# Optimization experiments

Measured on AMD Instinct MI355X. Metric: run time of the kernel, lower is better.

## Reference

```python
import jax, jax.numpy as jnp
import numpy as np

B, T, D, U = 64, 2048, 256, 256

def hard_sigmoid(x):
    return jnp.clip(0.2 * x + 0.5, 0.0, 1.0)

def setup_inputs() -> dict:
    key = jax.random.key(0)
    k1, k2, k3 = jax.random.split(key, 3)
    x = jax.random.normal(k1, (B, T, D), dtype=jnp.float32)
    kernel = jax.random.normal(k2, (D, 3 * U), dtype=jnp.float32) * (1.0 / np.sqrt(D))
    recurrent_kernel = jax.random.normal(k3, (U, 3 * U), dtype=jnp.float32) * (1.0 / np.sqrt(U))
    bias = jnp.zeros((3 * U,), dtype=jnp.float32)
    return {"x": x, "kernel": kernel, "recurrent_kernel": recurrent_kernel, "bias": bias}

def reference(x, kernel, recurrent_kernel, bias):
    # implementation=0 style: precompute input projections for all timesteps in one big matmul
    # x: [B,T,D], kernel: [D,3U] -> xz/xr/xh each [B,T,U]
    units = recurrent_kernel.shape[0]
    x_proj = jnp.einsum('btd,dh->bth', x, kernel) + bias  # [B,T,3U]
    xz, xr, xh = jnp.split(x_proj, 3, axis=-1)
    Uz = recurrent_kernel[:, :units]
    Ur = recurrent_kernel[:, units:2 * units]
    Uh = recurrent_kernel[:, 2 * units:]

    def step(h, xs):
        xz_t, xr_t, xh_t = xs  # each [B,U]
        z = hard_sigmoid(xz_t + h @ Uz)
        r = hard_sigmoid(xr_t + h @ Ur)
        hh = jnp.tanh(xh_t + (r * h) @ Uh)
        h_new = z * h + (1.0 - z) * hh
        return h_new, None

    h0 = jnp.zeros((x.shape[0], units), dtype=x.dtype)
    # scan over time: move T to leading axis
    xs = (jnp.swapaxes(xz, 0, 1), jnp.swapaxes(xr, 0, 1), jnp.swapaxes(xh, 0, 1))
    h_last, _ = jax.lax.scan(step, h0, xs)
    return h_last  # [B, U] (return_sequences=False)
```

## Files before the change

### kernel.cpp

```cpp
#include <hip/hip_runtime.h>


#define TB 2048
#define NU 256
#define G3 768

typedef __attribute__((ext_vector_type(8))) short bf16x8;
typedef __attribute__((ext_vector_type(4))) float f32x4;

__device__ inline unsigned short f2bf(float f){
  union{float f; unsigned u;} v; v.f = f;
  unsigned r = v.u + 0x7fffu + ((v.u >> 16) & 1u);
  return (unsigned short)(r >> 16);
}
__device__ inline unsigned pk2(float a, float b){
  return (unsigned)f2bf(a) | ((unsigned)f2bf(b) << 16);
}
__device__ inline float bflo(unsigned u){
  union{unsigned u; float f;} v; v.u = u << 16; return v.f;
}
__device__ inline float bfhi(unsigned u){
  union{unsigned u; float f;} v; v.u = u & 0xffff0000u; return v.f;
}
__device__ inline unsigned cvtpk(float a, float b){
  unsigned r;
  asm("v_cvt_pk_bf16_f32 %0, %1, %2" : "=v"(r) : "v"(a), "v"(b));
  return r;
}
__device__ inline float exp2_fast(float x){
#if __has_builtin(__builtin_amdgcn_exp2f)
  return __builtin_amdgcn_exp2f(x);
#else
  float r; asm("v_exp_f32 %0, %1" : "=v"(r) : "v"(x)); return r;
#endif
}

__global__ __launch_bounds__(256) void transpose_k(const float* __restrict__ W,
                                                   const float* __restrict__ R,
                                                   unsigned short* __restrict__ Wt,
                                                   unsigned short* __restrict__ Ut){
  int n = blockIdx.x;
  int k = threadIdx.x;
  if (n < G3) Wt[n*NU + k] = f2bf(W[k*G3 + n]);
  else        Ut[(n-G3)*NU + k] = f2bf(R[k*G3 + (n-G3)]);
}

__global__ __launch_bounds__(256) void proj_k(const float* __restrict__ x,
                                              const unsigned short* __restrict__ Wt,
                                              const float* __restrict__ bias,
                                              unsigned short* __restrict__ XA,
                                              unsigned short* __restrict__ XB){
  __shared__ short As[4096];
  __shared__ short Bs[4096];
  __shared__ short St[4096];
  const int tid  = threadIdx.x;
  const int lane = tid & 63;
  const int wv   = tid >> 6;
  const int wr   = wv >> 1, wc = wv & 1;
  const int q    = lane >> 4, r16 = lane & 15;
  const int tm   = blockIdx.x;
  const int bn   = blockIdx.y;

  f32x4 acc[2][2];
  #pragma unroll
  for (int a=0;a<2;a++)
    #pragma unroll
    for (int b=0;b<2;b++) acc[a][b] = {0.f,0.f,0.f,0.f};

  const int mA = tid >> 2, kq = tid & 3;
  const int kc32 = kq >> 1, q0 = (kq & 1) * 2;

  for (int kc0 = 0; kc0 < 256; kc0 += 64){
    {
      const float* src = x + (size_t)mA*(2048*256) + (size_t)tm*256 + kc0 + kq*16;
      float4 f0 = *(const float4*)(src);
      float4 f1 = *(const float4*)(src+4);
      float4 f2 = *(const float4*)(src+8);
      float4 f3 = *(const float4*)(src+12);
      *(uint2*)&As[kc32*2048 + q0*512     + mA*8 + 0] = make_uint2(pk2(f0.x,f0.y), pk2(f0.z,f0.w));
      *(uint2*)&As[kc32*2048 + q0*512     + mA*8 + 4] = make_uint2(pk2(f1.x,f1.y), pk2(f1.z,f1.w));
      *(uint2*)&As[kc32*2048 + (q0+1)*512 + mA*8 + 0] = make_uint2(pk2(f2.x,f2.y), pk2(f2.z,f2.w));
      *(uint2*)&As[kc32*2048 + (q0+1)*512 + mA*8 + 4] = make_uint2(pk2(f3.x,f3.y), pk2(f3.z,f3.w));
    }
    {
      const unsigned short* srcB = Wt + (size_t)(bn*64 + mA)*256 + kc0 + kq*16;
      uint4 b0v = *(const uint4*)(srcB);
      uint4 b1v = *(const uint4*)(srcB+8);
      *(uint4*)&Bs[kc32*2048 + q0*512     + mA*8] = b0v;
      *(uint4*)&Bs[kc32*2048 + (q0+1)*512 + mA*8] = b1v;
    }
    __syncthreads();
    #pragma unroll
    for (int kk = 0; kk < 2; kk++){
      bf16x8 av[2], bv[2];
      #pragma unroll
      for (int rt=0; rt<2; rt++)
        av[rt] = *(const bf16x8*)&As[kk*2048 + q*512 + (wr*32+rt*16+r16)*8];
      #pragma unroll
      for (int ct=0; ct<2; ct++)
        bv[ct] = *(const bf16x8*)&Bs[kk*2048 + q*512 + (wc*32+ct*16+r16)*8];
      #pragma unroll
      for (int rt=0; rt<2; rt++)
        #pragma unroll
        for (int ct=0; ct<2; ct++)
          acc[rt][ct] = __builtin_amdgcn_mfma_f32_16x16x32_bf16(av[rt], bv[ct], acc[rt][ct], 0,0,0);
    }
    __syncthreads();
  }

  const int csub = (bn < 4) ? 0 : (bn < 8 ? 256 : 512);
  #pragma unroll
  for (int rt=0; rt<2; rt++){
    #pragma unroll
    for (int ct=0; ct<2; ct++){
      int colg = bn*64 + wc*32 + ct*16 + r16;
      float bb = bias[colg];
      int c = colg - csub;
      int wi = (c >> 5) & 1, tt2 = (c >> 4) & 1, r16g = c & 15;
      #pragma unroll
      for (int i=0;i<4;i++){
        int b = wr*32 + rt*16 + q*4 + i;
        int gg = b >> 4, lb = b & 15;
        int lane_ = (lb >> 2)*16 + r16g, ii = lb & 3;
        St[(gg*2+wi)*512 + lane_*8 + tt2*4 + ii] = (short)f2bf(acc[rt][ct][i] + bb);
      }
    }
  }
  __syncthreads();

  #pragma unroll
  for (int it=0; it<2; it++){
    int idx = tid + it*256;
    int chunk = idx >> 6, within = idx & 63;
    int gg = chunk >> 1, wi = chunk & 1;
    int w_ = (bn & 3)*2 + wi;
    uint4 val = *(const uint4*)&St[chunk*512 + within*8];
    if (bn < 8){
      int sel = (bn < 4) ? 0 : 1;
      *((uint4*)XA + ((((size_t)tm*4+gg)*8 + w_)*64 + within)*2 + sel) = val;
    } else {
      *((uint4*)XB + (((size_t)tm*4+gg)*8 + w_)*64 + within) = val;
    }
  }
}

__global__ __launch_bounds__(512, 2) void gru_k(const unsigned short* __restrict__ XA,
                                                const unsigned short* __restrict__ XB,
                                                const unsigned short* __restrict__ Ut,
                                                float* __restrict__ out){
  __shared__ short fb[8192];

  const int tid  = threadIdx.x;
  const int w    = tid >> 6;
  const int lane = tid & 63;
  const int q    = lane >> 4, r16 = lane & 15;
  const int g    = blockIdx.x;
  const int b0   = g * 16;

  const int lswz = (lane & ~3) | ((lane & 3) ^ ((((lane >> 4) & 1) << 1) | ((lane >> 3) & 1)));
  const int ix   = ((r16 >> 3) << 1) | ((lane >> 5) & 1);
  const int wrb  = w*512 + (r16 >> 3)*128 + q*32 + (r16 & 7);

  for (int i = tid; i < 8192; i += 512) fb[i] = 0;

  bf16x8 Uz[2][8], Ur[2][8], Uh[2][8];
  #pragma unroll
  for (int tt=0; tt<2; tt++){
    int cz = w*32 + tt*16 + r16;
    #pragma unroll
    for (int kc=0; kc<8; kc++){
      Uz[tt][kc] = *(const bf16x8*)&Ut[(cz      )*256 + kc*32 + q*8];
      Ur[tt][kc] = *(const bf16x8*)&Ut[(cz + 256)*256 + kc*32 + q*8];
      Uh[tt][kc] = *(const bf16x8*)&Ut[(cz + 512)*256 + kc*32 + q*8];
    }
  }

  float hprev[2][4] = {{0.f,0.f,0.f,0.f},{0.f,0.f,0.f,0.f}};

  const uint4* pA = (const uint4*)XA + ((size_t)(g*8+w)*64 + lane)*2;
  const uint4* pB = (const uint4*)XB + ((size_t)(g*8+w)*64 + lane);

  uint4 xa0 = pA[0], xa1 = pA[1];
  uint4 xb0 = pB[0];
  pA += 4096; pB += 2048;

  __syncthreads();

  #pragma unroll 1
  for (int t = 0; t < TB; t++){
    uint4 na0 = pA[0], na1 = pA[1];
    uint4 nb0 = pB[0];
    pA += 4096; pB += 2048;

    unsigned xw[8] = {xa0.x,xa0.y,xa0.z,xa0.w,xa1.x,xa1.y,xa1.z,xa1.w};

    f32x4 az[2], ar[2];
    #pragma unroll
    for (int tt=0; tt<2; tt++){
      #pragma unroll
      for (int i=0;i<4;i++){
        int s  = tt*4 + i;
        int sr = 8 + s;
        az[tt][i] = (s&1)  ? bfhi(xw[s>>1])  : bflo(xw[s>>1]);
        ar[tt][i] = (sr&1) ? bfhi(xw[sr>>1]) : bflo(xw[sr>>1]);
      }
    }
    #pragma unroll
    for (int kc=0; kc<8; kc++){
      bf16x8 a = *(const bf16x8*)&fb[kc*512 + lswz*8];
      ar[0] = __builtin_amdgcn_mfma_f32_16x16x32_bf16(a, Ur[0][kc], ar[0], 0,0,0);
      ar[1] = __builtin_amdgcn_mfma_f32_16x16x32_bf16(a, Ur[1][kc], ar[1], 0,0,0);
      az[0] = __builtin_amdgcn_mfma_f32_16x16x32_bf16(a, Uz[0][kc], az[0], 0,0,0);
      az[1] = __builtin_amdgcn_mfma_f32_16x16x32_bf16(a, Uz[1][kc], az[1], 0,0,0);
    }
    #pragma unroll
    for (int tt=0; tt<2; tt++){
      #pragma unroll
      for (int i=0;i<4;i++){
        float rr = __builtin_amdgcn_fmed3f(fmaf(0.2f, ar[tt][i], 0.5f), 0.f, 1.f);
        float v  = rr * hprev[tt][i];
        fb[4096 + wrb + tt*256 + ((i^ix)<<3)] = (short)cvtpk(v, v);
      }
    }
    __syncthreads();

    f32x4 ah[2];
    {
      unsigned xwb[4] = {xb0.x,xb0.y,xb0.z,xb0.w};
      #pragma unroll
      for (int ct=0; ct<2; ct++){
        #pragma unroll
        for (int i=0;i<4;i++){
          int s = ct*4 + i;
          ah[ct][i] = (s&1) ? bfhi(xwb[s>>1]) : bflo(xwb[s>>1]);
        }
      }
    }
    #pragma unroll
    for (int kc=0; kc<8; kc++){
      bf16x8 vv = *(const bf16x8*)&fb[4096 + kc*512 + lswz*8];
      ah[0] = __builtin_amdgcn_mfma_f32_16x16x32_bf16(vv, Uh[0][kc], ah[0], 0,0,0);
      ah[1] = __builtin_amdgcn_mfma_f32_16x16x32_bf16(vv, Uh[1][kc], ah[1], 0,0,0);
    }
    float z8[2][4];
    #pragma unroll
    for (int tt=0; tt<2; tt++)
      #pragma unroll
      for (int i=0;i<4;i++)
        z8[tt][i] = __builtin_amdgcn_fmed3f(fmaf(0.2f, az[tt][i], 0.5f), 0.f, 1.f);
    #pragma unroll
    for (int ct=0; ct<2; ct++){
      #pragma unroll
      for (int i=0;i<4;i++){
        float e  = exp2_fast(2.8853900817779268f * ah[ct][i]);
        float rc = __builtin_amdgcn_rcpf(e + 1.f);
        float hh = fmaf(-2.f, rc, 1.f);
        float hn = fmaf(z8[ct][i], hprev[ct][i] - hh, hh);
        hprev[ct][i] = hn;
        fb[wrb + ct*256 + ((i^ix)<<3)] = (short)cvtpk(hn, hn);
      }
    }
    __syncthreads();

    xa0 = na0; xa1 = na1; xb0 = nb0;
  }

  #pragma unroll
  for (int ct=0; ct<2; ct++)
    #pragma unroll
    for (int i=0;i<4;i++)
      out[(size_t)(b0 + q*4 + i)*256 + w*32 + ct*16 + r16] = hprev[ct][i];
}

extern "C" void kernel_launch(void* const* d_in, const int* in_sizes, int n_in,
                              void* d_out, int out_size, void* d_ws, size_t ws_size,
                              hipStream_t stream) {
  (void)in_sizes; (void)n_in; (void)out_size; (void)ws_size;
  const float* x    = (const float*)d_in[0];
  const float* Wk   = (const float*)d_in[1];
  const float* Rk   = (const float*)d_in[2];
  const float* bias = (const float*)d_in[3];
  float* out = (float*)d_out;

  unsigned short* XA = (unsigned short*)d_ws;
  unsigned short* XB = XA + (size_t)2048*32768;
  unsigned short* Wt = XB + (size_t)2048*16384;
  unsigned short* Ut = Wt + (size_t)768*256;

  hipLaunchKernelGGL(transpose_k, dim3(1536),    dim3(256), 0, stream, Wk, Rk, Wt, Ut);
  hipLaunchKernelGGL(proj_k,      dim3(2048,12), dim3(256), 0, stream, x, Wt, bias, XA, XB);
  hipLaunchKernelGGL(gru_k,       dim3(4),       dim3(512), 0, stream, XA, XB, Ut, out);
}
```

Before: 3.369 ms.

## Halve waves per GRU block and give each wave 64 output columns

The recurrent kernel now runs 4 waves per block instead of 8. Each wave owns 64 hidden units and keeps four column tiles of the Uz/Ur/Uh weights in registers, about 384 VGPRs. The aim is to cut barrier and LDS-read overhead per timestep, with one wave per SIMD issuing a longer, denser MFMA chain. The cost is heavy register pressure and less latency hiding, since no other wave shares each SIMD. The input-projection prefetch is also reordered so next-step loads are issued right after the current values are unpacked.

```diff
diff --git a/kernel.cpp b/kernel.cpp
--- a/kernel.cpp
+++ b/kernel.cpp
@@ -144,14 +144,14 @@
   }
 }
 
-__global__ __launch_bounds__(512, 2) void gru_k(const unsigned short* __restrict__ XA,
+__global__ __launch_bounds__(256, 1) void gru_k(const unsigned short* __restrict__ XA,
                                                 const unsigned short* __restrict__ XB,
                                                 const unsigned short* __restrict__ Ut,
                                                 float* __restrict__ out){
   __shared__ short fb[8192];
 
   const int tid  = threadIdx.x;
-  const int w    = tid >> 6;
+  const int w2   = tid >> 6;
   const int lane = tid & 63;
   const int q    = lane >> 4, r16 = lane & 15;
   const int g    = blockIdx.x;
@@ -159,14 +159,14 @@
 
   const int lswz = (lane & ~3) | ((lane & 3) ^ ((((lane >> 4) & 1) << 1) | ((lane >> 3) & 1)));
   const int ix   = ((r16 >> 3) << 1) | ((lane >> 5) & 1);
-  const int wrb  = w*512 + (r16 >> 3)*128 + q*32 + (r16 & 7);
-
-  for (int i = tid; i < 8192; i += 512) fb[i] = 0;
-
-  bf16x8 Uz[2][8], Ur[2][8], Uh[2][8];
-  #pragma unroll
-  for (int tt=0; tt<2; tt++){
-    int cz = w*32 + tt*16 + r16;
+  const int wrb  = w2*1024 + (r16 >> 3)*128 + q*32 + (r16 & 7);
+
+  for (int i = tid; i < 8192; i += 256) fb[i] = 0;
+
+  bf16x8 Uz[4][8], Ur[4][8], Uh[4][8];
+  #pragma unroll
+  for (int tt=0; tt<4; tt++){
+    int cz = w2*64 + tt*16 + r16;
     #pragma unroll
     for (int kc=0; kc<8; kc++){
       Uz[tt][kc] = *(const bf16x8*)&Ut[(cz      )*256 + kc*32 + q*8];
@@ -175,46 +175,48 @@
     }
   }
 
-  float hprev[2][4] = {{0.f,0.f,0.f,0.f},{0.f,0.f,0.f,0.f}};
-
-  const uint4* pA = (const uint4*)XA + ((size_t)(g*8+w)*64 + lane)*2;
-  const uint4* pB = (const uint4*)XB + ((size_t)(g*8+w)*64 + lane);
-
-  uint4 xa0 = pA[0], xa1 = pA[1];
-  uint4 xb0 = pB[0];
+  float hprev[4][4] = {{0,0,0,0},{0,0,0,0},{0,0,0,0},{0,0,0,0}};
+
+  const uint4* pA = (const uint4*)XA + ((size_t)(g*8 + 2*w2)*64 + lane)*2;
+  const uint4* pB = (const uint4*)XB + ((size_t)(g*8 + 2*w2)*64 + lane);
+
+  uint4 xa0 = pA[0], xa1 = pA[1], xa2 = pA[128], xa3 = pA[129];
+  uint4 xb0 = pB[0], xb1 = pB[64];
   pA += 4096; pB += 2048;
 
   __syncthreads();
 
   #pragma unroll 1
   for (int t = 0; t < TB; t++){
-    uint4 na0 = pA[0], na1 = pA[1];
-    uint4 nb0 = pB[0];
-    pA += 4096; pB += 2048;
-
-    unsigned xw[8] = {xa0.x,xa0.y,xa0.z,xa0.w,xa1.x,xa1.y,xa1.z,xa1.w};
-
-    f32x4 az[2], ar[2];
-    #pragma unroll
-    for (int tt=0; tt<2; tt++){
-      #pragma unroll
-      for (int i=0;i<4;i++){
-        int s  = tt*4 + i;
-        int sr = 8 + s;
-        az[tt][i] = (s&1)  ? bfhi(xw[s>>1])  : bflo(xw[s>>1]);
-        ar[tt][i] = (sr&1) ? bfhi(xw[sr>>1]) : bflo(xw[sr>>1]);
-      }
-    }
+    f32x4 az[4], ar[4];
+    {
+      unsigned zw[8] = {xa0.x,xa0.y,xa0.z,xa0.w, xa2.x,xa2.y,xa2.z,xa2.w};
+      unsigned rw[8] = {xa1.x,xa1.y,xa1.z,xa1.w, xa3.x,xa3.y,xa3.z,xa3.w};
+      #pragma unroll
+      for (int tt=0; tt<4; tt++){
+        #pragma unroll
+        for (int i=0;i<4;i++){
+          unsigned uz = zw[tt*2 + (i>>1)];
+          unsigned ur = rw[tt*2 + (i>>1)];
+          az[tt][i] = (i&1) ? bfhi(uz) : bflo(uz);
+          ar[tt][i] = (i&1) ? bfhi(ur) : bflo(ur);
+        }
+      }
+    }
+    xa0 = pA[0]; xa1 = pA[1]; xa2 = pA[128]; xa3 = pA[129];
+    pA += 4096;
+
     #pragma unroll
     for (int kc=0; kc<8; kc++){
       bf16x8 a = *(const bf16x8*)&fb[kc*512 + lswz*8];
-      ar[0] = __builtin_amdgcn_mfma_f32_16x16x32_bf16(a, Ur[0][kc], ar[0], 0,0,0);
-      ar[1] = __builtin_amdgcn_mfma_f32_16x16x32_bf16(a, Ur[1][kc], ar[1], 0,0,0);
-      az[0] = __builtin_amdgcn_mfma_f32_16x16x32_bf16(a, Uz[0][kc], az[0], 0,0,0);
-      az[1] = __builtin_amdgcn_mfma_f32_16x16x32_bf16(a, Uz[1][kc], az[1], 0,0,0);
-    }
-    #pragma unroll
-    for (int tt=0; tt<2; tt++){
+      #pragma unroll
+      for (int tt=0; tt<4; tt++){
+        ar[tt] = __builtin_amdgcn_mfma_f32_16x16x32_bf16(a, Ur[tt][kc], ar[tt], 0,0,0);
+        az[tt] = __builtin_amdgcn_mfma_f32_16x16x32_bf16(a, Uz[tt][kc], az[tt], 0,0,0);
+      }
+    }
+    #pragma unroll
+    for (int tt=0; tt<4; tt++){
       #pragma unroll
       for (int i=0;i<4;i++){
         float rr = __builtin_amdgcn_fmed3f(fmaf(0.2f, ar[tt][i], 0.5f), 0.f, 1.f);
@@ -224,32 +226,35 @@
     }
     __syncthreads();
 
-    f32x4 ah[2];
-    {
-      unsigned xwb[4] = {xb0.x,xb0.y,xb0.z,xb0.w};
-      #pragma unroll
-      for (int ct=0; ct<2; ct++){
+    f32x4 ah[4];
+    {
+      unsigned hw_[8] = {xb0.x,xb0.y,xb0.z,xb0.w, xb1.x,xb1.y,xb1.z,xb1.w};
+      #pragma unroll
+      for (int tt=0; tt<4; tt++)
         #pragma unroll
         for (int i=0;i<4;i++){
-          int s = ct*4 + i;
-          ah[ct][i] = (s&1) ? bfhi(xwb[s>>1]) : bflo(xwb[s>>1]);
+          unsigned uh = hw_[tt*2 + (i>>1)];
+          ah[tt][i] = (i&1) ? bfhi(uh) : bflo(uh);
         }
-      }
-    }
+    }
+    xb0 = pB[0]; xb1 = pB[64];
+    pB += 2048;
+
     #pragma unroll
     for (int kc=0; kc<8; kc++){
       bf16x8 vv = *(const bf16x8*)&fb[4096 + kc*512 + lswz*8];
-      ah[0] = __builtin_amdgcn_mfma_f32_16x16x32_bf16(vv, Uh[0][kc], ah[0], 0,0,0);
-      ah[1] = __builtin_amdgcn_mfma_f32_16x16x32_bf16(vv, Uh[1][kc], ah[1], 0,0,0);
-    }
-    float z8[2][4];
-    #pragma unroll
-    for (int tt=0; tt<2; tt++)
+      #pragma unroll
+      for (int tt=0; tt<4; tt++)
+        ah[tt] = __builtin_amdgcn_mfma_f32_16x16x32_bf16(vv, Uh[tt][kc], ah[tt], 0,0,0);
+    }
+    float z8[4][4];
+    #pragma unroll
+    for (int tt=0; tt<4; tt++)
       #pragma unroll
       for (int i=0;i<4;i++)
         z8[tt][i] = __builtin_amdgcn_fmed3f(fmaf(0.2f, az[tt][i], 0.5f), 0.f, 1.f);
     #pragma unroll
-    for (int ct=0; ct<2; ct++){
+    for (int ct=0; ct<4; ct++){
       #pragma unroll
       for (int i=0;i<4;i++){
         float e  = exp2_fast(2.8853900817779268f * ah[ct][i]);
@@ -261,15 +266,13 @@
       }
     }
     __syncthreads();
-
-    xa0 = na0; xa1 = na1; xb0 = nb0;
-  }
-
-  #pragma unroll
-  for (int ct=0; ct<2; ct++)
+  }
+
+  #pragma unroll
+  for (int ct=0; ct<4; ct++)
     #pragma unroll
     for (int i=0;i<4;i++)
-      out[(size_t)(b0 + q*4 + i)*256 + w*32 + ct*16 + r16] = hprev[ct][i];
+      out[(size_t)(b0 + q*4 + i)*256 + w2*64 + ct*16 + r16] = hprev[ct][i];
 }
 
 extern "C" void kernel_launch(void* const* d_in, const int* in_sizes, int n_in,
@@ -289,5 +292,5 @@
 
   hipLaunchKernelGGL(transpose_k, dim3(1536),    dim3(256), 0, stream, Wk, Rk, Wt, Ut);
   hipLaunchKernelGGL(proj_k,      dim3(2048,12), dim3(256), 0, stream, x, Wt, bias, XA, XB);
-  hipLaunchKernelGGL(gru_k,       dim3(4),       dim3(512), 0, stream, XA, XB, Ut, out);
-}
+  hipLaunchKernelGGL(gru_k,       dim3(4),       dim3(256), 0, stream, XA, XB, Ut, out);
+}
```

After: 5.313 ms. 57.7% more time.
